# Kernel tuning notes

Hardware: AMD Instinct MI355X
Metric: run time of the kernel (lower is better)

The kernel has to match this reference:

```python
import jax, jax.numpy as jnp
import numpy as np

B, T, S, D = 16, 64, 256, 512
NEG_INF = -1e9  # finite stand-in for -inf mask fill (identical sparsemax output, autodiff-safe)


def sparsemax(z, axis=-1):
    # sparsemax(z) = clip(z - tau, 0), tau from sorted cumsum threshold
    z = z - jnp.max(z, axis=axis, keepdims=True)
    z_srt = -jnp.sort(-z, axis=axis)                      # descending sort
    z_cum = jnp.cumsum(z_srt, axis=axis) - 1.0
    k = jnp.arange(1, z.shape[axis] + 1, dtype=z.dtype)   # rho = 1..d
    support = (k * z_srt) > z_cum
    supp_size = jnp.sum(support, axis=axis, keepdims=True)
    tau = jnp.take_along_axis(z_cum, supp_size - 1, axis=axis) / supp_size.astype(z.dtype)
    return jnp.clip(z - tau, 0.0)


def setup_inputs() -> dict:
    key = jax.random.key(0)
    ks = jax.random.split(key, 9)
    init = lambda k, shape: (jax.random.normal(k, shape, jnp.float32) * 0.05)
    return {
        "source": jax.random.normal(ks[0], (B, T, D), jnp.float32),
        "memory_bank": jax.random.normal(ks[1], (B, S, D), jnp.float32),
        "memory_mask": jax.random.randint(ks[2], (B, S), 0, 2).astype(jnp.int32),
        "W_q": init(ks[3], (D, D)),   # linear_query weight
        "b_q": init(ks[4], (D,)),     # linear_query bias
        "W_c": init(ks[5], (D, D)),   # linear_context weight (no bias)
        "v": init(ks[6], (D,)),       # v projection (dim -> 1)
        "W_out": init(ks[7], (D, 2 * D)),  # linear_out weight
        "b_out": init(ks[8], (D,)),        # linear_out bias (mlp path has bias)
    }


def reference(source, memory_bank, memory_mask, W_q, b_q, W_c, v, W_out, b_out):
    # MLP (Bahdanau) score: v^T tanh(W_q q + U_c h)
    wq = jnp.einsum('btd,ed->bte', source, W_q) + b_q        # (B,T,D)
    uh = jnp.einsum('bsd,ed->bse', memory_bank, W_c)         # (B,S,D)
    wquh = jnp.tanh(wq[:, :, None, :] + uh[:, None, :, :])   # (B,T,S,D) big intermediate
    align = jnp.einsum('btsd,d->bts', wquh, v)               # (B,T,S)
    align = jnp.where(memory_mask[:, None, :].astype(bool), align, NEG_INF)
    align_vectors = sparsemax(align, axis=-1)                # (B,T,S)
    c = jnp.einsum('bts,bsd->btd', align_vectors, memory_bank)
    concat_c = jnp.concatenate([c, source], axis=-1)         # (B,T,2D)
    attn_h = jnp.einsum('btf,df->btd', concat_c, W_out) + b_out  # no tanh on mlp path
    return attn_h.transpose(1, 0, 2), align_vectors.transpose(1, 0, 2)
```

## Files before the change

kernel.cpp:

```cpp
#include <hip/hip_runtime.h>
#include <hip/hip_bf16.h>

#define BB 16
#define TT 64
#define SS 256
#define DD 512

typedef __bf16 bf16x8 __attribute__((ext_vector_type(8)));
typedef float f32x4 __attribute__((ext_vector_type(4)));

__device__ __forceinline__ ushort f2b(float x) {
    __hip_bfloat16 h = __float2bfloat16(x);
    return __builtin_bit_cast(ushort, h);
}
__device__ __forceinline__ float b2f(ushort u) {
    unsigned int x = (unsigned int)u << 16;
    return __builtin_bit_cast(float, x);
}

#define S_SRC (BB * TT * DD)
#define S_MB  (BB * SS * DD)
#define S_WQ  (DD * DD)
#define S_WC  (DD * DD)
#define S_WO  (DD * 2 * DD)

__global__ __launch_bounds__(256) void cast_all(
    const float* __restrict__ src, const float* __restrict__ mb,
    const float* __restrict__ wq, const float* __restrict__ wc,
    const float* __restrict__ wo,
    ushort* __restrict__ src_b, ushort* __restrict__ mb_b,
    ushort* __restrict__ wq_b, ushort* __restrict__ wc_b,
    ushort* __restrict__ wo_b) {
    int g = blockIdx.x * 256 + threadIdx.x;
    const int G0 = S_SRC / 4, G1 = S_MB / 4, G2 = S_WQ / 4, G3 = S_WC / 4;
    const float* in;
    ushort* out;
    int local;
    if (g < G0) { in = src; out = src_b; local = g; }
    else if (g < G0 + G1) { in = mb; out = mb_b; local = g - G0; }
    else if (g < G0 + G1 + G2) { in = wq; out = wq_b; local = g - G0 - G1; }
    else if (g < G0 + G1 + G2 + G3) { in = wc; out = wc_b; local = g - G0 - G1 - G2; }
    else { in = wo; out = wo_b; local = g - G0 - G1 - G2 - G3; }
    float4 x = *(const float4*)(in + (size_t)local * 4);
    ushort4 y = {f2b(x.x), f2b(x.y), f2b(x.z), f2b(x.w)};
    *(ushort4*)(out + (size_t)local * 4) = y;
}

__global__ __launch_bounds__(256) void mega_gemm(
    const ushort* __restrict__ src_b, const ushort* __restrict__ mb_b,
    const ushort* __restrict__ wqw_b, const ushort* __restrict__ wcw_b,
    const ushort* __restrict__ wo_b,
    const float* __restrict__ b_q, const float* __restrict__ b_out,
    float* __restrict__ Ewq, float* __restrict__ Y,
    ushort* __restrict__ EuT, ushort* __restrict__ M2) {
    __shared__ ushort Asm[64 * 72];
    __shared__ ushort Bsm[64 * 72];
    const int id = blockIdx.x;
    const ushort* Ab;
    const ushort* Bb;
    const float* bias = nullptr;
    void* Cp;
    int ldb, N, m0, n0;
    bool exp2x, obf16, hasb;
    size_t coff = 0;
    if (id < 256) {
        const bool isY = id >= 128;
        const int l = id & 127;
        m0 = (l >> 3) * 64; n0 = (l & 7) * 64;
        Ab = src_b;
        Bb = isY ? (wo_b + DD) : wqw_b;
        ldb = isY ? 2 * DD : DD;
        bias = isY ? b_out : b_q;
        hasb = true; exp2x = !isY; obf16 = false; N = DD;
        Cp = isY ? (void*)Y : (void*)Ewq;
    } else if (id < 768) {
        const int l = id - 256;
        const int bz = l >> 5, tl = l & 31;
        m0 = (tl >> 2) * 64; n0 = (tl & 3) * 64;
        Ab = wcw_b;
        Bb = mb_b + (size_t)bz * SS * DD;
        ldb = DD;
        hasb = false; exp2x = true; obf16 = true; N = SS;
        Cp = (void*)EuT; coff = (size_t)bz * DD * SS;
    } else {
        const int l = id - 768;
        const int bz = l >> 5, tl = l & 31;
        m0 = (tl >> 3) * 64; n0 = (tl & 7) * 64;
        Ab = mb_b + (size_t)bz * SS * DD;
        Bb = wo_b;
        ldb = 2 * DD;
        hasb = false; exp2x = false; obf16 = true; N = DD;
        Cp = (void*)M2; coff = (size_t)bz * SS * DD;
    }

    const int tid = threadIdx.x;
    const int lane = tid & 63;
    const int wave = tid >> 6;
    const int wm = wave & 1, wn = wave >> 1;

    const int srow = tid >> 3;
    const int schunk = tid & 7;
    const ushort* Ag0 = Ab + (size_t)(m0 + srow) * DD + schunk * 8;
    const ushort* Ag1 = Ag0 + (size_t)32 * DD;
    const ushort* Bg0 = Bb + (size_t)(n0 + srow) * ldb + schunk * 8;
    const ushort* Bg1 = Bg0 + (size_t)32 * ldb;
    const int lw = srow * 72 + schunk * 8;

    const int l15 = lane & 15, quad = lane >> 4;
    const int ar = (wm * 32 + l15) * 72 + quad * 8;
    const int br = (wn * 32 + l15) * 72 + quad * 8;

    f32x4 acc00 = {0.f, 0.f, 0.f, 0.f}, acc01 = {0.f, 0.f, 0.f, 0.f};
    f32x4 acc10 = {0.f, 0.f, 0.f, 0.f}, acc11 = {0.f, 0.f, 0.f, 0.f};

    uint4 a0 = *(const uint4*)Ag0;
    uint4 a1 = *(const uint4*)Ag1;
    uint4 b0 = *(const uint4*)Bg0;
    uint4 b1 = *(const uint4*)Bg1;
    const int P = DD >> 6;
    for (int p = 0; p < P; ++p) {
        __syncthreads();
        *(uint4*)&Asm[lw] = a0;
        *(uint4*)&Asm[lw + 32 * 72] = a1;
        *(uint4*)&Bsm[lw] = b0;
        *(uint4*)&Bsm[lw + 32 * 72] = b1;
        __syncthreads();
        if (p + 1 < P) {
            int ko = (p + 1) << 6;
            a0 = *(const uint4*)(Ag0 + ko);
            a1 = *(const uint4*)(Ag1 + ko);
            b0 = *(const uint4*)(Bg0 + ko);
            b1 = *(const uint4*)(Bg1 + ko);
        }
        bf16x8 fa0 = *(const bf16x8*)&Asm[ar];
        bf16x8 fa1 = *(const bf16x8*)&Asm[ar + 16 * 72];
        bf16x8 fb0 = *(const bf16x8*)&Bsm[br];
        bf16x8 fb1 = *(const bf16x8*)&Bsm[br + 16 * 72];
        acc00 = __builtin_amdgcn_mfma_f32_16x16x32_bf16(fa0, fb0, acc00, 0, 0, 0);
        acc01 = __builtin_amdgcn_mfma_f32_16x16x32_bf16(fa0, fb1, acc01, 0, 0, 0);
        acc10 = __builtin_amdgcn_mfma_f32_16x16x32_bf16(fa1, fb0, acc10, 0, 0, 0);
        acc11 = __builtin_amdgcn_mfma_f32_16x16x32_bf16(fa1, fb1, acc11, 0, 0, 0);
        fa0 = *(const bf16x8*)&Asm[ar + 32];
        fa1 = *(const bf16x8*)&Asm[ar + 16 * 72 + 32];
        fb0 = *(const bf16x8*)&Bsm[br + 32];
        fb1 = *(const bf16x8*)&Bsm[br + 16 * 72 + 32];
        acc00 = __builtin_amdgcn_mfma_f32_16x16x32_bf16(fa0, fb0, acc00, 0, 0, 0);
        acc01 = __builtin_amdgcn_mfma_f32_16x16x32_bf16(fa0, fb1, acc01, 0, 0, 0);
        acc10 = __builtin_amdgcn_mfma_f32_16x16x32_bf16(fa1, fb0, acc10, 0, 0, 0);
        acc11 = __builtin_amdgcn_mfma_f32_16x16x32_bf16(fa1, fb1, acc11, 0, 0, 0);
    }
    const int nA = n0 + wn * 32 + l15;
    float bias0 = 0.f, bias1 = 0.f;
    if (hasb) { bias0 = bias[nA]; bias1 = bias[nA + 16]; }
    float* Cf = (float*)Cp;
    ushort* Cb = (ushort*)Cp;
#pragma unroll
    for (int mt = 0; mt < 2; ++mt) {
        f32x4 accN0 = mt ? acc10 : acc00;
        f32x4 accN1 = mt ? acc11 : acc01;
#pragma unroll
        for (int r = 0; r < 4; ++r) {
            int m = m0 + wm * 32 + mt * 16 + quad * 4 + r;
            float v0 = accN0[r] + bias0;
            float v1 = accN1[r] + bias1;
            if (exp2x) { v0 = __expf(2.0f * v0); v1 = __expf(2.0f * v1); }
            size_t i0 = coff + (size_t)m * N + nA;
            if (obf16) { Cb[i0] = f2b(v0); Cb[i0 + 16] = f2b(v1); }
            else { Cf[i0] = v0; Cf[i0 + 16] = v1; }
        }
    }
}

__global__ __launch_bounds__(256) void align5(const float* __restrict__ Ewq,
                                              const ushort* __restrict__ EuT,
                                              const int* __restrict__ mask,
                                              const float* __restrict__ v,
                                              const ushort* __restrict__ M2,
                                              const float* __restrict__ Y,
                                              float* __restrict__ align_out,
                                              float* __restrict__ out0) {
    const int tg = blockIdx.x, b = blockIdx.y;
    const int t0 = tg * 2, t1 = t0 + 1;
    const int bt0 = b * TT + t0, bt1 = bt0 + 1;
    const int tid = threadIdx.x;
    const int lane = tid & 63;
    const int wave = tid >> 6;
    __shared__ float4 EL[DD];
    __shared__ float zs0[SS], zs1[SS];
    __shared__ float svp[4];
    __shared__ float4 cmb[2][128];
    __shared__ int lst0[SS], lst1[SS];
    __shared__ int cnt[2];

    if (tid < 2) cnt[tid] = 0;
    const float* E0p = Ewq + (size_t)bt0 * DD;
    const float* E1p = Ewq + (size_t)bt1 * DD;
    float pv = 0.f;
    for (int d = tid; d < DD; d += 256) {
        float vv = v[d];
        EL[d] = make_float4(E0p[d], E1p[d], vv, 0.f);
        pv += vv;
    }
#pragma unroll
    for (int off = 32; off > 0; off >>= 1) pv += __shfl_xor(pv, off, 64);
    if (lane == 0) svp[wave] = pv;
    __syncthreads();
    const float sv = svp[0] + svp[1] + svp[2] + svp[3];

    const ushort* U = EuT + (size_t)b * DD * SS + tid;
    float a0 = 0.f, a1 = 0.f;
#pragma unroll 16
    for (int d = 0; d < DD; ++d) {
        float u = b2f(U[(size_t)d * SS]);
        float4 el = EL[d];
        float den0 = __builtin_fmaf(el.x, u, 1.0f);
        float den1 = __builtin_fmaf(el.y, u, 1.0f);
        a0 = __builtin_fmaf(el.z, __builtin_amdgcn_rcpf(den0), a0);
        a1 = __builtin_fmaf(el.z, __builtin_amdgcn_rcpf(den1), a1);
    }
    int mk = mask[b * SS + tid];
    zs0[tid] = mk ? (sv - 2.0f * a0) : -1e9f;
    zs1[tid] = mk ? (sv - 2.0f * a1) : -1e9f;
    __syncthreads();

    if (wave < 2) {
        float* zz = wave ? zs1 : zs0;
        float z0 = zz[lane];
        float z1 = zz[lane + 64];
        float z2 = zz[lane + 128];
        float z3 = zz[lane + 192];
        float mx = fmaxf(fmaxf(z0, z1), fmaxf(z2, z3));
#pragma unroll
        for (int off = 32; off > 0; off >>= 1) mx = fmaxf(mx, __shfl_xor(mx, off, 64));
        z0 -= mx; z1 -= mx; z2 -= mx; z3 -= mx;
        float lo = -1.0f, hi = 0.0f;
        for (int it = 0; it < 24; ++it) {
            float mid = 0.5f * (lo + hi);
            float ssum = fmaxf(z0 - mid, 0.f) + fmaxf(z1 - mid, 0.f) +
                         fmaxf(z2 - mid, 0.f) + fmaxf(z3 - mid, 0.f);
#pragma unroll
            for (int off = 32; off > 0; off >>= 1) ssum += __shfl_xor(ssum, off, 64);
            if (ssum >= 1.0f) lo = mid; else hi = mid;
        }
        float tau = 0.5f * (lo + hi);
        zz[lane] = fmaxf(z0 - tau, 0.f);
        zz[lane + 64] = fmaxf(z1 - tau, 0.f);
        zz[lane + 128] = fmaxf(z2 - tau, 0.f);
        zz[lane + 192] = fmaxf(z3 - tau, 0.f);
    }
    __syncthreads();

    align_out[((size_t)t0 * BB + b) * SS + tid] = zs0[tid];
    align_out[((size_t)t1 * BB + b) * SS + tid] = zs1[tid];

    if (zs0[tid] > 0.f) lst0[atomicAdd(&cnt[0], 1)] = tid;
    if (zs1[tid] > 0.f) lst1[atomicAdd(&cnt[1], 1)] = tid;
    __syncthreads();
    const int n0c = cnt[0], n1c = cnt[1];

    const int ch = tid & 127, sg = tid >> 7;
    const ushort* M2b = M2 + (size_t)b * SS * DD + ch * 4;
    float4 at0 = {0.f, 0.f, 0.f, 0.f}, at1 = {0.f, 0.f, 0.f, 0.f};
#pragma unroll 4
    for (int j = sg; j < n0c; j += 2) {
        int s = lst0[j];
        float p = zs0[s];
        ushort4 m4 = *(const ushort4*)(M2b + (size_t)s * DD);
        at0.x = __builtin_fmaf(p, b2f(m4.x), at0.x);
        at0.y = __builtin_fmaf(p, b2f(m4.y), at0.y);
        at0.z = __builtin_fmaf(p, b2f(m4.z), at0.z);
        at0.w = __builtin_fmaf(p, b2f(m4.w), at0.w);
    }
#pragma unroll 4
    for (int j = sg; j < n1c; j += 2) {
        int s = lst1[j];
        float p = zs1[s];
        ushort4 m4 = *(const ushort4*)(M2b + (size_t)s * DD);
        at1.x = __builtin_fmaf(p, b2f(m4.x), at1.x);
        at1.y = __builtin_fmaf(p, b2f(m4.y), at1.y);
        at1.z = __builtin_fmaf(p, b2f(m4.z), at1.z);
        at1.w = __builtin_fmaf(p, b2f(m4.w), at1.w);
    }
    if (sg == 1) { cmb[0][ch] = at0; cmb[1][ch] = at1; }
    __syncthreads();
    if (sg == 0) {
        float4 p0 = cmb[0][ch], p1 = cmb[1][ch];
        const float4* Y0 = (const float4*)(Y + (size_t)bt0 * DD);
        const float4* Y1 = (const float4*)(Y + (size_t)bt1 * DD);
        float4 y0 = Y0[ch], y1 = Y1[ch];
        float4 o0, o1;
        o0.x = at0.x + p0.x + y0.x; o0.y = at0.y + p0.y + y0.y;
        o0.z = at0.z + p0.z + y0.z; o0.w = at0.w + p0.w + y0.w;
        o1.x = at1.x + p1.x + y1.x; o1.y = at1.y + p1.y + y1.y;
        o1.z = at1.z + p1.z + y1.z; o1.w = at1.w + p1.w + y1.w;
        float4* O0 = (float4*)(out0 + ((size_t)t0 * BB + b) * DD);
        float4* O1 = (float4*)(out0 + ((size_t)t1 * BB + b) * DD);
        O0[ch] = o0;
        O1[ch] = o1;
    }
}

extern "C" void kernel_launch(void* const* d_in, const int* in_sizes, int n_in,
                              void* d_out, int out_size, void* d_ws, size_t ws_size,
                              hipStream_t stream) {
    const float* source = (const float*)d_in[0];
    const float* memory_bank = (const float*)d_in[1];
    const int* memory_mask = (const int*)d_in[2];
    const float* W_q = (const float*)d_in[3];
    const float* b_q = (const float*)d_in[4];
    const float* W_c = (const float*)d_in[5];
    const float* v = (const float*)d_in[6];
    const float* W_out = (const float*)d_in[7];
    const float* b_out = (const float*)d_in[8];

    float* out0 = (float*)d_out;
    float* out1 = out0 + (size_t)TT * BB * DD;

    float* Ewq = (float*)d_ws;
    float* Y = Ewq + S_SRC;
    ushort* EuT = (ushort*)(Y + S_SRC);
    ushort* M2 = EuT + S_MB;
    ushort* src_b = M2 + S_MB;
    ushort* mb_b = src_b + S_SRC;
    ushort* wqw_b = mb_b + S_MB;
    ushort* wcw_b = wqw_b + S_WQ;
    ushort* wo_b = wcw_b + S_WC;

    dim3 blk(256);
    int ngroups = (S_SRC + S_MB + S_WQ + S_WC + S_WO) / 4;
    cast_all<<<dim3(ngroups / 256), blk, 0, stream>>>(
        source, memory_bank, W_q, W_c, W_out, src_b, mb_b, wqw_b, wcw_b, wo_b);
    mega_gemm<<<dim3(1280), blk, 0, stream>>>(
        src_b, mb_b, wqw_b, wcw_b, wo_b, b_q, b_out, Ewq, Y, EuT, M2);
    align5<<<dim3(TT / 2, BB), blk, 0, stream>>>(
        Ewq, EuT, memory_mask, v, M2, Y, out1, out0);
}
```

Baseline: 125.5 us.

## Use direct global-to-LDS loads with swizzle and store Eu row-major for vector reads

```diff
diff --git a/kernel.cpp b/kernel.cpp
--- a/kernel.cpp
+++ b/kernel.cpp
@@ -16,6 +16,11 @@
 __device__ __forceinline__ float b2f(ushort u) {
     unsigned int x = (unsigned int)u << 16;
     return __builtin_bit_cast(float, x);
+}
+__device__ __forceinline__ void gload16(const ushort* g, ushort* l) {
+    __builtin_amdgcn_global_load_lds(
+        (const __attribute__((address_space(1))) unsigned int*)g,
+        (__attribute__((address_space(3))) unsigned int*)l, 16, 0, 0);
 }
 
 #define S_SRC (BB * TT * DD)
@@ -48,13 +53,13 @@
 
 __global__ __launch_bounds__(256) void mega_gemm(
     const ushort* __restrict__ src_b, const ushort* __restrict__ mb_b,
-    const ushort* __restrict__ wqw_b, const ushort* __restrict__ wcw_b,
+    const ushort* __restrict__ wq_b, const ushort* __restrict__ wc_b,
     const ushort* __restrict__ wo_b,
     const float* __restrict__ b_q, const float* __restrict__ b_out,
     float* __restrict__ Ewq, float* __restrict__ Y,
-    ushort* __restrict__ EuT, ushort* __restrict__ M2) {
-    __shared__ ushort Asm[64 * 72];
-    __shared__ ushort Bsm[64 * 72];
+    ushort* __restrict__ Eu, ushort* __restrict__ M2) {
+    __shared__ ushort Asm[64 * 64];
+    __shared__ ushort Bsm[64 * 64];
     const int id = blockIdx.x;
     const ushort* Ab;
     const ushort* Bb;
@@ -68,7 +73,7 @@
         const int l = id & 127;
         m0 = (l >> 3) * 64; n0 = (l & 7) * 64;
         Ab = src_b;
-        Bb = isY ? (wo_b + DD) : wqw_b;
+        Bb = isY ? (wo_b + DD) : wq_b;
         ldb = isY ? 2 * DD : DD;
         bias = isY ? b_out : b_q;
         hasb = true; exp2x = !isY; obf16 = false; N = DD;
@@ -76,12 +81,12 @@
     } else if (id < 768) {
         const int l = id - 256;
         const int bz = l >> 5, tl = l & 31;
-        m0 = (tl >> 2) * 64; n0 = (tl & 3) * 64;
-        Ab = wcw_b;
-        Bb = mb_b + (size_t)bz * SS * DD;
+        m0 = (tl >> 3) * 64; n0 = (tl & 7) * 64;
+        Ab = mb_b + (size_t)bz * SS * DD;
+        Bb = wc_b;
         ldb = DD;
-        hasb = false; exp2x = true; obf16 = true; N = SS;
-        Cp = (void*)EuT; coff = (size_t)bz * DD * SS;
+        hasb = false; exp2x = true; obf16 = true; N = DD;
+        Cp = (void*)Eu; coff = (size_t)bz * SS * DD;
     } else {
         const int l = id - 768;
         const int bz = l >> 5, tl = l & 31;
@@ -98,52 +103,48 @@
     const int wave = tid >> 6;
     const int wm = wave & 1, wn = wave >> 1;
 
-    const int srow = tid >> 3;
-    const int schunk = tid & 7;
-    const ushort* Ag0 = Ab + (size_t)(m0 + srow) * DD + schunk * 8;
-    const ushort* Ag1 = Ag0 + (size_t)32 * DD;
-    const ushort* Bg0 = Bb + (size_t)(n0 + srow) * ldb + schunk * 8;
-    const ushort* Bg1 = Bg0 + (size_t)32 * ldb;
-    const int lw = srow * 72 + schunk * 8;
+    const int rl = lane >> 3;
+    const int csw = (lane & 7) ^ rl;
+    const ushort* Ag0 = Ab + (size_t)(m0 + wave * 16 + rl) * DD + csw * 8;
+    const ushort* Ag1 = Ag0 + (size_t)8 * DD;
+    const ushort* Bg0 = Bb + (size_t)(n0 + wave * 16 + rl) * ldb + csw * 8;
+    const ushort* Bg1 = Bg0 + (size_t)8 * ldb;
+    ushort* Al0 = &Asm[(wave * 16) * 64];
+    ushort* Al1 = &Asm[(wave * 16 + 8) * 64];
+    ushort* Bl0 = &Bsm[(wave * 16) * 64];
+    ushort* Bl1 = &Bsm[(wave * 16 + 8) * 64];
 
     const int l15 = lane & 15, quad = lane >> 4;
-    const int ar = (wm * 32 + l15) * 72 + quad * 8;
-    const int br = (wn * 32 + l15) * 72 + quad * 8;
+    const int xr = l15 & 7;
+    const int arow0 = (wm * 32 + l15) * 64, arow1 = arow0 + 16 * 64;
+    const int brow0 = (wn * 32 + l15) * 64, brow1 = brow0 + 16 * 64;
+    const int c0 = (quad ^ xr) * 8;
+    const int c1 = ((4 + quad) ^ xr) * 8;
 
     f32x4 acc00 = {0.f, 0.f, 0.f, 0.f}, acc01 = {0.f, 0.f, 0.f, 0.f};
     f32x4 acc10 = {0.f, 0.f, 0.f, 0.f}, acc11 = {0.f, 0.f, 0.f, 0.f};
 
-    uint4 a0 = *(const uint4*)Ag0;
-    uint4 a1 = *(const uint4*)Ag1;
-    uint4 b0 = *(const uint4*)Bg0;
-    uint4 b1 = *(const uint4*)Bg1;
     const int P = DD >> 6;
     for (int p = 0; p < P; ++p) {
+        const int ko = p << 6;
         __syncthreads();
-        *(uint4*)&Asm[lw] = a0;
-        *(uint4*)&Asm[lw + 32 * 72] = a1;
-        *(uint4*)&Bsm[lw] = b0;
-        *(uint4*)&Bsm[lw + 32 * 72] = b1;
+        gload16(Ag0 + ko, Al0);
+        gload16(Ag1 + ko, Al1);
+        gload16(Bg0 + ko, Bl0);
+        gload16(Bg1 + ko, Bl1);
         __syncthreads();
-        if (p + 1 < P) {
-            int ko = (p + 1) << 6;
-            a0 = *(const uint4*)(Ag0 + ko);
-            a1 = *(const uint4*)(Ag1 + ko);
-            b0 = *(const uint4*)(Bg0 + ko);
-            b1 = *(const uint4*)(Bg1 + ko);
-        }
-        bf16x8 fa0 = *(const bf16x8*)&Asm[ar];
-        bf16x8 fa1 = *(const bf16x8*)&Asm[ar + 16 * 72];
-        bf16x8 fb0 = *(const bf16x8*)&Bsm[br];
-        bf16x8 fb1 = *(const bf16x8*)&Bsm[br + 16 * 72];
+        bf16x8 fa0 = *(const bf16x8*)&Asm[arow0 + c0];
+        bf16x8 fa1 = *(const bf16x8*)&Asm[arow1 + c0];
+        bf16x8 fb0 = *(const bf16x8*)&Bsm[brow0 + c0];
+        bf16x8 fb1 = *(const bf16x8*)&Bsm[brow1 + c0];
         acc00 = __builtin_amdgcn_mfma_f32_16x16x32_bf16(fa0, fb0, acc00, 0, 0, 0);
         acc01 = __builtin_amdgcn_mfma_f32_16x16x32_bf16(fa0, fb1, acc01, 0, 0, 0);
         acc10 = __builtin_amdgcn_mfma_f32_16x16x32_bf16(fa1, fb0, acc10, 0, 0, 0);
         acc11 = __builtin_amdgcn_mfma_f32_16x16x32_bf16(fa1, fb1, acc11, 0, 0, 0);
-        fa0 = *(const bf16x8*)&Asm[ar + 32];
-        fa1 = *(const bf16x8*)&Asm[ar + 16 * 72 + 32];
-        fb0 = *(const bf16x8*)&Bsm[br + 32];
-        fb1 = *(const bf16x8*)&Bsm[br + 16 * 72 + 32];
+        fa0 = *(const bf16x8*)&Asm[arow0 + c1];
+        fa1 = *(const bf16x8*)&Asm[arow1 + c1];
+        fb0 = *(const bf16x8*)&Bsm[brow0 + c1];
+        fb1 = *(const bf16x8*)&Bsm[brow1 + c1];
         acc00 = __builtin_amdgcn_mfma_f32_16x16x32_bf16(fa0, fb0, acc00, 0, 0, 0);
         acc01 = __builtin_amdgcn_mfma_f32_16x16x32_bf16(fa0, fb1, acc01, 0, 0, 0);
         acc10 = __builtin_amdgcn_mfma_f32_16x16x32_bf16(fa1, fb0, acc10, 0, 0, 0);
@@ -172,7 +173,7 @@
 }
 
 __global__ __launch_bounds__(256) void align5(const float* __restrict__ Ewq,
-                                              const ushort* __restrict__ EuT,
+                                              const ushort* __restrict__ Eu,
                                               const int* __restrict__ mask,
                                               const float* __restrict__ v,
                                               const ushort* __restrict__ M2,
@@ -207,16 +208,24 @@
     __syncthreads();
     const float sv = svp[0] + svp[1] + svp[2] + svp[3];
 
-    const ushort* U = EuT + (size_t)b * DD * SS + tid;
+    const ushort* U = Eu + ((size_t)b * SS + tid) * DD;
     float a0 = 0.f, a1 = 0.f;
-#pragma unroll 16
-    for (int d = 0; d < DD; ++d) {
-        float u = b2f(U[(size_t)d * SS]);
-        float4 el = EL[d];
-        float den0 = __builtin_fmaf(el.x, u, 1.0f);
-        float den1 = __builtin_fmaf(el.y, u, 1.0f);
-        a0 = __builtin_fmaf(el.z, __builtin_amdgcn_rcpf(den0), a0);
-        a1 = __builtin_fmaf(el.z, __builtin_amdgcn_rcpf(den1), a1);
+#pragma unroll 4
+    for (int d0 = 0; d0 < DD; d0 += 8) {
+        union { uint4 q; unsigned w[4]; } uw;
+        uw.q = *(const uint4*)(U + d0);
+#pragma unroll
+        for (int jj = 0; jj < 4; ++jj) {
+            unsigned wd = uw.w[jj];
+            float ulo = __builtin_bit_cast(float, wd << 16);
+            float uhi = __builtin_bit_cast(float, wd & 0xffff0000u);
+            float4 e0 = EL[d0 + jj * 2];
+            float4 e1 = EL[d0 + jj * 2 + 1];
+            a0 = __builtin_fmaf(e0.z, __builtin_amdgcn_rcpf(__builtin_fmaf(e0.x, ulo, 1.0f)), a0);
+            a1 = __builtin_fmaf(e0.z, __builtin_amdgcn_rcpf(__builtin_fmaf(e0.y, ulo, 1.0f)), a1);
+            a0 = __builtin_fmaf(e1.z, __builtin_amdgcn_rcpf(__builtin_fmaf(e1.x, uhi, 1.0f)), a0);
+            a1 = __builtin_fmaf(e1.z, __builtin_amdgcn_rcpf(__builtin_fmaf(e1.y, uhi, 1.0f)), a1);
+        }
     }
     int mk = mask[b * SS + tid];
     zs0[tid] = mk ? (sv - 2.0f * a0) : -1e9f;
@@ -234,7 +243,7 @@
         for (int off = 32; off > 0; off >>= 1) mx = fmaxf(mx, __shfl_xor(mx, off, 64));
         z0 -= mx; z1 -= mx; z2 -= mx; z3 -= mx;
         float lo = -1.0f, hi = 0.0f;
-        for (int it = 0; it < 24; ++it) {
+        for (int it = 0; it < 20; ++it) {
             float mid = 0.5f * (lo + hi);
             float ssum = fmaxf(z0 - mid, 0.f) + fmaxf(z1 - mid, 0.f) +
                          fmaxf(z2 - mid, 0.f) + fmaxf(z3 - mid, 0.f);
@@ -318,8 +327,8 @@
 
     float* Ewq = (float*)d_ws;
     float* Y = Ewq + S_SRC;
-    ushort* EuT = (ushort*)(Y + S_SRC);
-    ushort* M2 = EuT + S_MB;
+    ushort* Eu = (ushort*)(Y + S_SRC);
+    ushort* M2 = Eu + S_MB;
     ushort* src_b = M2 + S_MB;
     ushort* mb_b = src_b + S_SRC;
     ushort* wqw_b = mb_b + S_MB;
@@ -331,7 +340,7 @@
     cast_all<<<dim3(ngroups / 256), blk, 0, stream>>>(
         source, memory_bank, W_q, W_c, W_out, src_b, mb_b, wqw_b, wcw_b, wo_b);
     mega_gemm<<<dim3(1280), blk, 0, stream>>>(
-        src_b, mb_b, wqw_b, wcw_b, wo_b, b_q, b_out, Ewq, Y, EuT, M2);
+        src_b, mb_b, wqw_b, wcw_b, wo_b, b_q, b_out, Ewq, Y, Eu, M2);
     align5<<<dim3(TT / 2, BB), blk, 0, stream>>>(
-        Ewq, EuT, memory_mask, v, M2, Y, out1, out0);
-}
+        Ewq, Eu, memory_mask, v, M2, Y, out1, out0);
+}
```

Measured after the change: 123.0 us. 1.02x faster.
